# Optimization experiments

Measured on AMD Instinct MI355X. Metric: run time of the kernel, lower is better.

## Reference

```python
import jax, jax.numpy as jnp
import numpy as np

T, B, F, H = 2048, 256, 64, 128


def setup_inputs() -> dict:
    key = jax.random.key(0)
    ks = jax.random.split(key, 6)
    s_i = 1.0 / np.sqrt(F)
    s_h = 1.0 / np.sqrt(H)
    x = jax.random.normal(ks[0], (T, B, F), dtype=jnp.float32)
    # flax GRUCell params: input kernels ir/iz/in (with bias), hidden kernels
    # hr/hz (no bias), hn (with bias). Packed as [r | z | n].
    Wi = jax.random.normal(ks[1], (F, 3 * H), dtype=jnp.float32) * s_i
    bi = jnp.zeros((3 * H,), dtype=jnp.float32)
    Whrz = jax.random.normal(ks[2], (H, 2 * H), dtype=jnp.float32) * s_h  # hr | hz
    Whn = jax.random.normal(ks[3], (H, H), dtype=jnp.float32) * s_h
    bn = jnp.zeros((H,), dtype=jnp.float32)
    return {"x": x, "Wi": Wi, "bi": bi, "Whrz": Whrz, "Whn": Whn, "bn": bn}


def reference(x, Wi, bi, Whrz, Whn, bn):
    # Faithful flax nn.RNN(nn.GRUCell(H), time_major=True) with zero init carry.
    # r = sigmoid(x@Wir + bir + h@Whr)
    # z = sigmoid(x@Wiz + biz + h@Whz)
    # h' = (1 - z) * n + z * h
    Tn, Bn, _ = x.shape
    Hn = Whn.shape[0]
    # Precompute all input projections in one big GEMM (same math, vectorized over time).
    xg = jnp.einsum("tbf,fg->tbg", x, Wi) + bi  # [T, B, 3H]

    def step(h, xg_t):
        hrz = h @ Whrz  # [B, 2H]
        r = jax.nn.sigmoid(xg_t[..., :Hn] + hrz[..., :Hn])
        z = jax.nn.sigmoid(xg_t[..., Hn:2 * Hn] + hrz[..., Hn:])
        n = jnp.tanh(xg_t[..., 2 * Hn:] + r * (h @ Whn + bn))
        h_new = (1.0 - z) * n + z * h
        return h_new, h_new

    h0 = jnp.zeros((Bn, Hn), dtype=x.dtype)
    _, ys = jax.lax.scan(step, h0, xg)
    return ys  # [T, B, H] — all hidden states, as nn.RNN returns
```

## Files before the change

kernel.cpp:

```cpp
#include <hip/hip_runtime.h>

#define TT 2048
#define BB 256
#define FF 64
#define HH 128
#define NT 512
#define MR 4
#define NBLK (BB / MR)
#define RS (BB * FF / 4)
#define HSTR 320

typedef _Float16 half8 __attribute__((ext_vector_type(8)));
typedef _Float16 half4 __attribute__((ext_vector_type(4)));
typedef float    f32x4 __attribute__((ext_vector_type(4)));

#if __has_builtin(__builtin_amdgcn_rcpf)
#define FRCP(v) __builtin_amdgcn_rcpf(v)
#else
#define FRCP(v) (1.0f / (v))
#endif

__device__ __forceinline__ f32x4 mf(f32x4 a, f32x4 b, f32x4 c) {
  return __builtin_amdgcn_mfma_f32_16x16x32_f16(
      __builtin_bit_cast(half8, a), __builtin_bit_cast(half8, b), c, 0, 0, 0);
}

__device__ __forceinline__ void step_barrier() {
  asm volatile("s_waitcnt lgkmcnt(0)" ::: "memory");
  __builtin_amdgcn_s_barrier();
  __builtin_amdgcn_sched_barrier(0);
}

__global__ void __launch_bounds__(NT)
__attribute__((amdgpu_waves_per_eu(2, 2)))
gru_scan_kernel(const float* __restrict__ x,
                const float* __restrict__ Wi,
                const float* __restrict__ bi,
                const float* __restrict__ Whrz,
                const float* __restrict__ Whn,
                const float* __restrict__ bn,
                float* __restrict__ out)
{
  const int tid   = threadIdx.x;
  const int w     = tid >> 6;
  const int l     = tid & 63;
  const int n16   = l & 15;
  const int q     = l >> 4;
  const int u     = 16 * w + n16;
  const int rr    = n16 & 3;
  const int brow0 = blockIdx.x * MR;

  __shared__ __align__(16) char h_lds[2][MR * HSTR];
  __shared__ __align__(16) char x_lds[4][MR * HSTR];

  f32x4 Bhr[4], Bhz[4], Bhn2[4];
  f32x4 Bxr[2], Bxz[2], Bxn2[2];
  #pragma unroll
  for (int kt = 0; kt < 4; ++kt) {
    half8 fr, fz, fn;
    #pragma unroll
    for (int j = 0; j < 8; ++j) {
      const int k = 32 * kt + 8 * q + j;
      fr[j] = (_Float16)Whrz[(size_t)k * 256 + u];
      fz[j] = (_Float16)Whrz[(size_t)k * 256 + 128 + u];
      fn[j] = (_Float16)Whn[(size_t)k * 128 + u];
    }
    Bhr[kt]  = __builtin_bit_cast(f32x4, fr);
    Bhz[kt]  = __builtin_bit_cast(f32x4, fz);
    Bhn2[kt] = __builtin_bit_cast(f32x4, fn);
  }
  #pragma unroll
  for (int kt = 0; kt < 2; ++kt) {
    half8 fr, fz, fn;
    #pragma unroll
    for (int j = 0; j < 8; ++j) {
      const int k = 32 * kt + 8 * q + j;
      fr[j] = (_Float16)Wi[(size_t)k * 384 + u];
      fz[j] = (_Float16)Wi[(size_t)k * 384 + 128 + u];
      fn[j] = (_Float16)Wi[(size_t)k * 384 + 256 + u];
    }
    Bxr[kt]  = __builtin_bit_cast(f32x4, fr);
    Bxz[kt]  = __builtin_bit_cast(f32x4, fz);
    Bxn2[kt] = __builtin_bit_cast(f32x4, fn);
  }
  const float bR = bi[u], bZ = bi[128 + u], bX = bi[256 + u], bH = bn[u];
  const f32x4 biasR = f32x4{bR, bR, bR, bR};
  const f32x4 biasZ = f32x4{bZ, bZ, bZ, bZ};
  const f32x4 biasX = f32x4{bX, bX, bX, bX};
  const f32x4 biasH = f32x4{bH, bH, bH, bH};

  int hA[4], xA[2];
  #pragma unroll
  for (int kt = 0; kt < 4; ++kt) hA[kt] = rr * HSTR + kt * 64 + q * 16;
  #pragma unroll
  for (int kt = 0; kt < 2; ++kt) xA[kt] = rr * HSTR + kt * 64 + q * 16;

  const int hW = q * HSTR + 2 * u;

  const bool loader = (tid < 64);
  const int  srow   = tid >> 4;
  const int  sc     = tid & 15;
  const int  sbyte  = srow * HSTR + sc * 8;

  if (loader) {
    *(f32x4*)(h_lds[0] + srow * HSTR + sc * 16) = f32x4{0.f, 0.f, 0.f, 0.f};
    #pragma unroll
    for (int s = 0; s < 2; ++s) {
      const float4 v =
          *(const float4*)(x + ((size_t)s * BB + brow0 + srow) * FF + sc * 4);
      half4 hf;
      hf[0] = (_Float16)v.x; hf[1] = (_Float16)v.y;
      hf[2] = (_Float16)v.z; hf[3] = (_Float16)v.w;
      *(half4*)(x_lds[s] + sbyte) = hf;
    }
  }
  const float4* xsrc =
      (const float4*)(x + ((size_t)2 * BB + brow0 + srow) * FF + sc * 4);
  float4 xva, xvb;
  if (loader) {
    xva = xsrc[0];
    xvb = xsrc[(size_t)RS];
    xsrc += 2 * (size_t)RS;
  }

  float h_old = 0.0f;
  float* outp = out + ((size_t)brow0 + q) * HH + u;
  __syncthreads();

#define STEP(P, XV)                                                         \
  {                                                                         \
    const int t_ = tbase + (P);                                             \
    const char* hb = h_lds[(P) & 1];                                        \
    const char* xb = x_lds[(P) & 3];                                        \
    f32x4 Ah0 = *(const f32x4*)(hb + hA[0]);                                \
    f32x4 Ah1 = *(const f32x4*)(hb + hA[1]);                                \
    f32x4 Ah2 = *(const f32x4*)(hb + hA[2]);                                \
    f32x4 Ah3 = *(const f32x4*)(hb + hA[3]);                                \
    f32x4 Ax0 = *(const f32x4*)(xb + xA[0]);                                \
    f32x4 Ax1 = *(const f32x4*)(xb + xA[1]);                                \
    if (loader) {                                                           \
      if (t_ + 2 < TT) {                                                    \
        half4 hf;                                                           \
        hf[0] = (_Float16)XV.x; hf[1] = (_Float16)XV.y;                     \
        hf[2] = (_Float16)XV.z; hf[3] = (_Float16)XV.w;                     \
        *(half4*)(x_lds[((P) + 2) & 3] + sbyte) = hf;           \
      }                                                                     \
      if (t_ + 4 < TT) { XV = *xsrc; xsrc += RS; }              \
    }                                                                       \
    f32x4 Cr = mf(Ah0, Bhr[0], biasR);                                      \
    Cr = mf(Ah1, Bhr[1], Cr); Cr = mf(Ah2, Bhr[2], Cr);                     \
    Cr = mf(Ah3, Bhr[3], Cr);                                               \
    Cr = mf(Ax0, Bxr[0], Cr); Cr = mf(Ax1, Bxr[1], Cr);                     \
    f32x4 Cz = mf(Ah0, Bhz[0], biasZ);                                      \
    Cz = mf(Ah1, Bhz[1], Cz); Cz = mf(Ah2, Bhz[2], Cz);                     \
    Cz = mf(Ah3, Bhz[3], Cz);                                               \
    Cz = mf(Ax0, Bxz[0], Cz); Cz = mf(Ax1, Bxz[1], Cz);                     \
    f32x4 Chn = mf(Ah0, Bhn2[0], biasH);                                    \
    Chn = mf(Ah1, Bhn2[1], Chn); Chn = mf(Ah2, Bhn2[2], Chn);               \
    Chn = mf(Ah3, Bhn2[3], Chn);                                            \
    f32x4 Cxn = mf(Ax0, Bxn2[0], biasX);                                    \
    Cxn = mf(Ax1, Bxn2[1], Cxn);                                            \
    \
    \
    const float cr  = (q < 2) ? ((q == 0) ? Cr[0]  : Cr[1])                 \
                              : ((q == 2) ? Cr[2]  : Cr[3]);                \
    const float cz  = (q < 2) ? ((q == 0) ? Cz[0]  : Cz[1])                 \
                              : ((q == 2) ? Cz[2]  : Cz[3]);                \
    const float chn = (q < 2) ? ((q == 0) ? Chn[0] : Chn[1])                \
                              : ((q == 2) ? Chn[2] : Chn[3]);               \
    const float cxn = (q < 2) ? ((q == 0) ? Cxn[0] : Cxn[1])                \
                              : ((q == 2) ? Cxn[2] : Cxn[3]);               \
    const float A_ = __expf(-cr);                                           \
    const float rg = FRCP(1.0f + A_);                                       \
    const float B_ = __expf(-cz);                                           \
    const float na = cxn + rg * chn;                                        \
    const float E_ = __expf(2.0f * na);                                     \
    const float Ep1 = E_ + 1.0f;                                            \
    const float num = h_old * Ep1 + B_ * (E_ - 1.0f);                       \
    const float hv  = num * FRCP(Ep1 * (1.0f + B_));                        \
    h_old = hv;                                                             \
    *(_Float16*)(h_lds[((P) + 1) & 1] + hW) = (_Float16)hv;                 \
    *outp = hv;                                                             \
    outp += (size_t)BB * HH;                                                \
    step_barrier();                                                         \
  }

  for (int tbase = 0; tbase < TT; tbase += 4) {
    STEP(0, xva)
    STEP(1, xvb)
    STEP(2, xva)
    STEP(3, xvb)
  }
#undef STEP
}

extern "C" void kernel_launch(void* const* d_in, const int* in_sizes, int n_in,
                              void* d_out, int out_size, void* d_ws, size_t ws_size,
                              hipStream_t stream) {
  const float* x    = (const float*)d_in[0];
  const float* Wi   = (const float*)d_in[1];
  const float* bi   = (const float*)d_in[2];
  const float* Whrz = (const float*)d_in[3];
  const float* Whn  = (const float*)d_in[4];
  const float* bn   = (const float*)d_in[5];
  float* out = (float*)d_out;

  gru_scan_kernel<<<dim3(NBLK), dim3(NT), 0, stream>>>(
      x, Wi, bi, Whrz, Whn, bn, out);
}
```

Measured before the change: 893.7 us.

## Process eight batch rows per block with two MFMA tiles per wave

Doubles the batch rows handled per block from 4 to 8, so each wave runs two sets of MFMA chains and gate computations per timestep. The grid halves to 32 blocks, and each block pays its per-step barrier and weight-load setup once for twice the work. Biases move from the MFMA accumulator init into the scalar gate math, so the accumulators start at zero. The trade is a longer serial critical path per step and fewer CUs in use, which only pays off if the latency is hidden by interleaving the two independent MFMA chains.

After: 1.720 ms. 92.5% more time.

```diff
diff --git a/kernel.cpp b/kernel.cpp
--- a/kernel.cpp
+++ b/kernel.cpp
@@ -5,7 +5,7 @@
 #define FF 64
 #define HH 128
 #define NT 512
-#define MR 4
+#define MR 8
 #define NBLK (BB / MR)
 #define RS (BB * FF / 4)
 #define HSTR 320
@@ -84,26 +84,23 @@
     Bxn2[kt] = __builtin_bit_cast(f32x4, fn);
   }
   const float bR = bi[u], bZ = bi[128 + u], bX = bi[256 + u], bH = bn[u];
-  const f32x4 biasR = f32x4{bR, bR, bR, bR};
-  const f32x4 biasZ = f32x4{bZ, bZ, bZ, bZ};
-  const f32x4 biasX = f32x4{bX, bX, bX, bX};
-  const f32x4 biasH = f32x4{bH, bH, bH, bH};
+  const f32x4 Zf = f32x4{0.f, 0.f, 0.f, 0.f};
 
   int hA[4], xA[2];
   #pragma unroll
   for (int kt = 0; kt < 4; ++kt) hA[kt] = rr * HSTR + kt * 64 + q * 16;
   #pragma unroll
   for (int kt = 0; kt < 2; ++kt) xA[kt] = rr * HSTR + kt * 64 + q * 16;
-
-  const int hW = q * HSTR + 2 * u;
-
-  const bool loader = (tid < 64);
+  const int hWA = q * HSTR + 2 * u;
+  const int hWB = (q + 4) * HSTR + 2 * u;
+
+  const bool loader = (tid < 128);
   const int  srow   = tid >> 4;
   const int  sc     = tid & 15;
   const int  sbyte  = srow * HSTR + sc * 8;
 
   if (loader) {
-    *(f32x4*)(h_lds[0] + srow * HSTR + sc * 16) = f32x4{0.f, 0.f, 0.f, 0.f};
+    *(f32x4*)(h_lds[0] + srow * HSTR + sc * 16) = Zf;
     #pragma unroll
     for (int s = 0; s < 2; ++s) {
       const float4 v =
@@ -123,21 +120,64 @@
     xsrc += 2 * (size_t)RS;
   }
 
-  float h_old = 0.0f;
-  float* outp = out + ((size_t)brow0 + q) * HH + u;
+  float h_oldA = 0.0f;
+  float h_oldB = 0.0f;
+  float* outpA = out + ((size_t)brow0 + q) * HH + u;
+  float* outpB = outpA + 4 * HH;
   __syncthreads();
+
+#define SEL(C_) ((q < 2) ? ((q == 0) ? (C_)[0] : (C_)[1])                   \
+                         : ((q == 2) ? (C_)[2] : (C_)[3]))
+#define GATE(cr_, cz_, chn_, cxn_, hold_, hdst_, hW_, outp_)                \
+  {                                                                         \
+    const float A_ = __expf(-((cr_) + bR));                                 \
+    const float rg = FRCP(1.0f + A_);                                       \
+    const float B_ = __expf(-((cz_) + bZ));                                 \
+    const float na = ((cxn_) + bX) + rg * ((chn_) + bH);                    \
+    const float E_ = __expf(2.0f * na);                                     \
+    const float Ep1 = E_ + 1.0f;                                            \
+    const float num = (hold_) * Ep1 + B_ * (E_ - 1.0f);                     \
+    const float hv  = num * FRCP(Ep1 * (1.0f + B_));                        \
+    (hold_) = hv;                                                           \
+    *(_Float16*)((hdst_) + (hW_)) = (_Float16)hv;                           \
+    *(outp_) = hv;                                                          \
+  }
+
+#define GEMM(Ah0, Ah1, Ah2, Ah3, Ax0, Ax1, Cr, Cz, Chn, Cxn)               \
+    f32x4 Cr = mf(Ah0, Bhr[0], Zf);                                         \
+    Cr = mf(Ah1, Bhr[1], Cr); Cr = mf(Ah2, Bhr[2], Cr);                     \
+    Cr = mf(Ah3, Bhr[3], Cr);                                               \
+    Cr = mf(Ax0, Bxr[0], Cr); Cr = mf(Ax1, Bxr[1], Cr);                     \
+    f32x4 Cz = mf(Ah0, Bhz[0], Zf);                                         \
+    Cz = mf(Ah1, Bhz[1], Cz); Cz = mf(Ah2, Bhz[2], Cz);                     \
+    Cz = mf(Ah3, Bhz[3], Cz);                                               \
+    Cz = mf(Ax0, Bxz[0], Cz); Cz = mf(Ax1, Bxz[1], Cz);                     \
+    f32x4 Chn = mf(Ah0, Bhn2[0], Zf);                                       \
+    Chn = mf(Ah1, Bhn2[1], Chn); Chn = mf(Ah2, Bhn2[2], Chn);               \
+    Chn = mf(Ah3, Bhn2[3], Chn);                                            \
+    f32x4 Cxn = mf(Ax0, Bxn2[0], Zf);                                       \
+    Cxn = mf(Ax1, Bxn2[1], Cxn);
 
 #define STEP(P, XV)                                                         \
   {                                                                         \
     const int t_ = tbase + (P);                                             \
     const char* hb = h_lds[(P) & 1];                                        \
     const char* xb = x_lds[(P) & 3];                                        \
-    f32x4 Ah0 = *(const f32x4*)(hb + hA[0]);                                \
-    f32x4 Ah1 = *(const f32x4*)(hb + hA[1]);                                \
-    f32x4 Ah2 = *(const f32x4*)(hb + hA[2]);                                \
-    f32x4 Ah3 = *(const f32x4*)(hb + hA[3]);                                \
-    f32x4 Ax0 = *(const f32x4*)(xb + xA[0]);                                \
-    f32x4 Ax1 = *(const f32x4*)(xb + xA[1]);                                \
+    char* hdst = h_lds[((P) + 1) & 1];                                      \
+                                          \
+    f32x4 aAh0 = *(const f32x4*)(hb + hA[0]);                               \
+    f32x4 aAh1 = *(const f32x4*)(hb + hA[1]);                               \
+    f32x4 aAh2 = *(const f32x4*)(hb + hA[2]);                               \
+    f32x4 aAh3 = *(const f32x4*)(hb + hA[3]);                               \
+    f32x4 aAx0 = *(const f32x4*)(xb + xA[0]);                               \
+    f32x4 aAx1 = *(const f32x4*)(xb + xA[1]);                               \
+                                          \
+    f32x4 bAh0 = *(const f32x4*)(hb + 4 * HSTR + hA[0]);                    \
+    f32x4 bAh1 = *(const f32x4*)(hb + 4 * HSTR + hA[1]);                    \
+    f32x4 bAh2 = *(const f32x4*)(hb + 4 * HSTR + hA[2]);                    \
+    f32x4 bAh3 = *(const f32x4*)(hb + 4 * HSTR + hA[3]);                    \
+    f32x4 bAx0 = *(const f32x4*)(xb + 4 * HSTR + xA[0]);                    \
+    f32x4 bAx1 = *(const f32x4*)(xb + 4 * HSTR + xA[1]);                    \
     if (loader) {                                                           \
       if (t_ + 2 < TT) {                                                    \
         half4 hf;                                                           \
@@ -147,41 +187,13 @@
       }                                                                     \
       if (t_ + 4 < TT) { XV = *xsrc; xsrc += RS; }              \
     }                                                                       \
-    f32x4 Cr = mf(Ah0, Bhr[0], biasR);                                      \
-    Cr = mf(Ah1, Bhr[1], Cr); Cr = mf(Ah2, Bhr[2], Cr);                     \
-    Cr = mf(Ah3, Bhr[3], Cr);                                               \
-    Cr = mf(Ax0, Bxr[0], Cr); Cr = mf(Ax1, Bxr[1], Cr);                     \
-    f32x4 Cz = mf(Ah0, Bhz[0], biasZ);                                      \
-    Cz = mf(Ah1, Bhz[1], Cz); Cz = mf(Ah2, Bhz[2], Cz);                     \
-    Cz = mf(Ah3, Bhz[3], Cz);                                               \
-    Cz = mf(Ax0, Bxz[0], Cz); Cz = mf(Ax1, Bxz[1], Cz);                     \
-    f32x4 Chn = mf(Ah0, Bhn2[0], biasH);                                    \
-    Chn = mf(Ah1, Bhn2[1], Chn); Chn = mf(Ah2, Bhn2[2], Chn);               \
-    Chn = mf(Ah3, Bhn2[3], Chn);                                            \
-    f32x4 Cxn = mf(Ax0, Bxn2[0], biasX);                                    \
-    Cxn = mf(Ax1, Bxn2[1], Cxn);                                            \
-    \
-    \
-    const float cr  = (q < 2) ? ((q == 0) ? Cr[0]  : Cr[1])                 \
-                              : ((q == 2) ? Cr[2]  : Cr[3]);                \
-    const float cz  = (q < 2) ? ((q == 0) ? Cz[0]  : Cz[1])                 \
-                              : ((q == 2) ? Cz[2]  : Cz[3]);                \
-    const float chn = (q < 2) ? ((q == 0) ? Chn[0] : Chn[1])                \
-                              : ((q == 2) ? Chn[2] : Chn[3]);               \
-    const float cxn = (q < 2) ? ((q == 0) ? Cxn[0] : Cxn[1])                \
-                              : ((q == 2) ? Cxn[2] : Cxn[3]);               \
-    const float A_ = __expf(-cr);                                           \
-    const float rg = FRCP(1.0f + A_);                                       \
-    const float B_ = __expf(-cz);                                           \
-    const float na = cxn + rg * chn;                                        \
-    const float E_ = __expf(2.0f * na);                                     \
-    const float Ep1 = E_ + 1.0f;                                            \
-    const float num = h_old * Ep1 + B_ * (E_ - 1.0f);                       \
-    const float hv  = num * FRCP(Ep1 * (1.0f + B_));                        \
-    h_old = hv;                                                             \
-    *(_Float16*)(h_lds[((P) + 1) & 1] + hW) = (_Float16)hv;                 \
-    *outp = hv;                                                             \
-    outp += (size_t)BB * HH;                                                \
+           \
+    GEMM(aAh0, aAh1, aAh2, aAh3, aAx0, aAx1, CrA, CzA, ChnA, CxnA)          \
+    GEMM(bAh0, bAh1, bAh2, bAh3, bAx0, bAx1, CrB, CzB, ChnB, CxnB)          \
+    GATE(SEL(CrA), SEL(CzA), SEL(ChnA), SEL(CxnA), h_oldA, hdst, hWA, outpA)\
+    GATE(SEL(CrB), SEL(CzB), SEL(ChnB), SEL(CxnB), h_oldB, hdst, hWB, outpB)\
+    outpA += (size_t)BB * HH;                                               \
+    outpB += (size_t)BB * HH;                                               \
     step_barrier();                                                         \
   }
 
@@ -192,6 +204,9 @@
     STEP(3, xvb)
   }
 #undef STEP
+#undef GEMM
+#undef GATE
+#undef SEL
 }
 
 extern "C" void kernel_launch(void* const* d_in, const int* in_sizes, int n_in,
```

## Load x fragments directly into registers and reorder MFMAs to start with input projection

Applied to the files above, without the earlier changes.

Removes the LDS staging of x, where one wave loaded, converted and stored x tiles for the whole block. Each lane now loads its own MFMA A-fragment of x straight from global memory two steps ahead and converts it with packed round-toward-zero f16 conversions. The MFMA chain is reordered so the x-projection products, which do not depend on the previous hidden state, are issued before the h-dependent ones and can overlap the LDS read of h. In exchange every wave issues redundant global loads of x, adds register pressure, and the conversion now rounds toward zero instead of to nearest.

Result: slower. 1.815 ms (+103.1%).

```diff
diff --git a/kernel.cpp b/kernel.cpp
--- a/kernel.cpp
+++ b/kernel.cpp
@@ -7,11 +7,10 @@
 #define NT 512
 #define MR 4
 #define NBLK (BB / MR)
-#define RS (BB * FF / 4)
 #define HSTR 320
 
 typedef _Float16 half8 __attribute__((ext_vector_type(8)));
-typedef _Float16 half4 __attribute__((ext_vector_type(4)));
+typedef __fp16   fp16x2 __attribute__((ext_vector_type(2)));
 typedef float    f32x4 __attribute__((ext_vector_type(4)));
 
 #if __has_builtin(__builtin_amdgcn_rcpf)
@@ -23,6 +22,15 @@
 __device__ __forceinline__ f32x4 mf(f32x4 a, f32x4 b, f32x4 c) {
   return __builtin_amdgcn_mfma_f32_16x16x32_f16(
       __builtin_bit_cast(half8, a), __builtin_bit_cast(half8, b), c, 0, 0, 0);
+}
+
+__device__ __forceinline__ f32x4 cvt8(const float4 a, const float4 b) {
+  union { fp16x2 h[4]; f32x4 v; } u;
+  u.h[0] = __builtin_amdgcn_cvt_pkrtz(a.x, a.y);
+  u.h[1] = __builtin_amdgcn_cvt_pkrtz(a.z, a.w);
+  u.h[2] = __builtin_amdgcn_cvt_pkrtz(b.x, b.y);
+  u.h[3] = __builtin_amdgcn_cvt_pkrtz(b.z, b.w);
+  return u.v;
 }
 
 __device__ __forceinline__ void step_barrier() {
@@ -51,7 +59,6 @@
   const int brow0 = blockIdx.x * MR;
 
   __shared__ __align__(16) char h_lds[2][MR * HSTR];
-  __shared__ __align__(16) char x_lds[4][MR * HSTR];
 
   f32x4 Bhr[4], Bhz[4], Bhn2[4];
   f32x4 Bxr[2], Bxz[2], Bxn2[2];
@@ -89,87 +96,80 @@
   const f32x4 biasX = f32x4{bX, bX, bX, bX};
   const f32x4 biasH = f32x4{bH, bH, bH, bH};
 
-  int hA[4], xA[2];
+  int hA[4];
   #pragma unroll
   for (int kt = 0; kt < 4; ++kt) hA[kt] = rr * HSTR + kt * 64 + q * 16;
-  #pragma unroll
-  for (int kt = 0; kt < 2; ++kt) xA[kt] = rr * HSTR + kt * 64 + q * 16;
-
   const int hW = q * HSTR + 2 * u;
 
-  const bool loader = (tid < 64);
-  const int  srow   = tid >> 4;
-  const int  sc     = tid & 15;
-  const int  sbyte  = srow * HSTR + sc * 8;
-
-  if (loader) {
-    *(f32x4*)(h_lds[0] + srow * HSTR + sc * 16) = f32x4{0.f, 0.f, 0.f, 0.f};
-    #pragma unroll
-    for (int s = 0; s < 2; ++s) {
-      const float4 v =
-          *(const float4*)(x + ((size_t)s * BB + brow0 + srow) * FF + sc * 4);
-      half4 hf;
-      hf[0] = (_Float16)v.x; hf[1] = (_Float16)v.y;
-      hf[2] = (_Float16)v.z; hf[3] = (_Float16)v.w;
-      *(half4*)(x_lds[s] + sbyte) = hf;
-    }
-  }
-  const float4* xsrc =
-      (const float4*)(x + ((size_t)2 * BB + brow0 + srow) * FF + sc * 4);
-  float4 xva, xvb;
-  if (loader) {
-    xva = xsrc[0];
-    xvb = xsrc[(size_t)RS];
-    xsrc += 2 * (size_t)RS;
+  const size_t xrow0 = ((size_t)brow0 + rr) * FF + q * 8;
+
+  if (tid < 64) {
+    *(f32x4*)(h_lds[0] + (tid >> 4) * HSTR + (tid & 15) * 16) =
+        f32x4{0.f, 0.f, 0.f, 0.f};
+  }
+  float4 rA0a, rA0b, rA1a, rA1b;
+  float4 rB0a, rB0b, rB1a, rB1b;
+  {
+    const float* p0 = x + xrow0;
+    rA0a = *(const float4*)(p0);
+    rA0b = *(const float4*)(p0 + 4);
+    rA1a = *(const float4*)(p0 + 32);
+    rA1b = *(const float4*)(p0 + 36);
+    const float* p1 = x + (size_t)BB * FF + xrow0;
+    rB0a = *(const float4*)(p1);
+    rB0b = *(const float4*)(p1 + 4);
+    rB1a = *(const float4*)(p1 + 32);
+    rB1b = *(const float4*)(p1 + 36);
   }
 
   float h_old = 0.0f;
   float* outp = out + ((size_t)brow0 + q) * HH + u;
   __syncthreads();
 
-#define STEP(P, XV)                                                         \
+#define SEL(C_) ((q < 2) ? ((q == 0) ? (C_)[0] : (C_)[1])                   \
+                         : ((q == 2) ? (C_)[2] : (C_)[3]))
+
+#define STEP(P, R0a, R0b, R1a, R1b)                                         \
   {                                                                         \
     const int t_ = tbase + (P);                                             \
     const char* hb = h_lds[(P) & 1];                                        \
-    const char* xb = x_lds[(P) & 3];                                        \
+    char* hdst = (char*)h_lds[((P) + 1) & 1];                               \
+             \
     f32x4 Ah0 = *(const f32x4*)(hb + hA[0]);                                \
     f32x4 Ah1 = *(const f32x4*)(hb + hA[1]);                                \
     f32x4 Ah2 = *(const f32x4*)(hb + hA[2]);                                \
     f32x4 Ah3 = *(const f32x4*)(hb + hA[3]);                                \
-    f32x4 Ax0 = *(const f32x4*)(xb + xA[0]);                                \
-    f32x4 Ax1 = *(const f32x4*)(xb + xA[1]);                                \
-    if (loader) {                                                           \
-      if (t_ + 2 < TT) {                                                    \
-        half4 hf;                                                           \
-        hf[0] = (_Float16)XV.x; hf[1] = (_Float16)XV.y;                     \
-        hf[2] = (_Float16)XV.z; hf[3] = (_Float16)XV.w;                     \
-        *(half4*)(x_lds[((P) + 2) & 3] + sbyte) = hf;           \
-      }                                                                     \
-      if (t_ + 4 < TT) { XV = *xsrc; xsrc += RS; }              \
+                     \
+    f32x4 Ax0 = cvt8(R0a, R0b);                                             \
+    f32x4 Ax1 = cvt8(R1a, R1b);                                             \
+               \
+    {                                                                       \
+      const int t2 = (t_ + 2 < TT) ? t_ + 2 : TT - 1;                       \
+      const float* p = x + (size_t)t2 * BB * FF + xrow0;                    \
+      R0a = *(const float4*)(p);                                            \
+      R0b = *(const float4*)(p + 4);                                        \
+      R1a = *(const float4*)(p + 32);                                       \
+      R1b = *(const float4*)(p + 36);                                       \
     }                                                                       \
-    f32x4 Cr = mf(Ah0, Bhr[0], biasR);                                      \
-    Cr = mf(Ah1, Bhr[1], Cr); Cr = mf(Ah2, Bhr[2], Cr);                     \
-    Cr = mf(Ah3, Bhr[3], Cr);                                               \
-    Cr = mf(Ax0, Bxr[0], Cr); Cr = mf(Ax1, Bxr[1], Cr);                     \
-    f32x4 Cz = mf(Ah0, Bhz[0], biasZ);                                      \
-    Cz = mf(Ah1, Bhz[1], Cz); Cz = mf(Ah2, Bhz[2], Cz);                     \
-    Cz = mf(Ah3, Bhz[3], Cz);                                               \
-    Cz = mf(Ax0, Bxz[0], Cz); Cz = mf(Ax1, Bxz[1], Cz);                     \
+            \
+    f32x4 Cr = mf(Ax0, Bxr[0], biasR);                                      \
+    Cr = mf(Ax1, Bxr[1], Cr);                                               \
+    f32x4 Cz = mf(Ax0, Bxz[0], biasZ);                                      \
+    Cz = mf(Ax1, Bxz[1], Cz);                                               \
+    f32x4 Cxn = mf(Ax0, Bxn2[0], biasX);                                    \
+    Cxn = mf(Ax1, Bxn2[1], Cxn);                                            \
+    Cr = mf(Ah0, Bhr[0], Cr); Cr = mf(Ah1, Bhr[1], Cr);                     \
+    Cr = mf(Ah2, Bhr[2], Cr); Cr = mf(Ah3, Bhr[3], Cr);                     \
+    Cz = mf(Ah0, Bhz[0], Cz); Cz = mf(Ah1, Bhz[1], Cz);                     \
+    Cz = mf(Ah2, Bhz[2], Cz); Cz = mf(Ah3, Bhz[3], Cz);                     \
     f32x4 Chn = mf(Ah0, Bhn2[0], biasH);                                    \
     Chn = mf(Ah1, Bhn2[1], Chn); Chn = mf(Ah2, Bhn2[2], Chn);               \
     Chn = mf(Ah3, Bhn2[3], Chn);                                            \
-    f32x4 Cxn = mf(Ax0, Bxn2[0], biasX);                                    \
-    Cxn = mf(Ax1, Bxn2[1], Cxn);                                            \
-    \
-    \
-    const float cr  = (q < 2) ? ((q == 0) ? Cr[0]  : Cr[1])                 \
-                              : ((q == 2) ? Cr[2]  : Cr[3]);                \
-    const float cz  = (q < 2) ? ((q == 0) ? Cz[0]  : Cz[1])                 \
-                              : ((q == 2) ? Cz[2]  : Cz[3]);                \
-    const float chn = (q < 2) ? ((q == 0) ? Chn[0] : Chn[1])                \
-                              : ((q == 2) ? Chn[2] : Chn[3]);               \
-    const float cxn = (q < 2) ? ((q == 0) ? Cxn[0] : Cxn[1])                \
-                              : ((q == 2) ? Cxn[2] : Cxn[3]);               \
+         \
+    const float cr  = SEL(Cr);                                              \
+    const float cz  = SEL(Cz);                                              \
+    const float chn = SEL(Chn);                                             \
+    const float cxn = SEL(Cxn);                                             \
     const float A_ = __expf(-cr);                                           \
     const float rg = FRCP(1.0f + A_);                                       \
     const float B_ = __expf(-cz);                                           \
@@ -179,19 +179,18 @@
     const float num = h_old * Ep1 + B_ * (E_ - 1.0f);                       \
     const float hv  = num * FRCP(Ep1 * (1.0f + B_));                        \
     h_old = hv;                                                             \
-    *(_Float16*)(h_lds[((P) + 1) & 1] + hW) = (_Float16)hv;                 \
+    *(_Float16*)(hdst + hW) = (_Float16)hv;                                 \
     *outp = hv;                                                             \
     outp += (size_t)BB * HH;                                                \
     step_barrier();                                                         \
   }
 
-  for (int tbase = 0; tbase < TT; tbase += 4) {
-    STEP(0, xva)
-    STEP(1, xvb)
-    STEP(2, xva)
-    STEP(3, xvb)
+  for (int tbase = 0; tbase < TT; tbase += 2) {
+    STEP(0, rA0a, rA0b, rA1a, rA1b)
+    STEP(1, rB0a, rB0b, rB1a, rB1b)
   }
 #undef STEP
+#undef SEL
 }
 
 extern "C" void kernel_launch(void* const* d_in, const int* in_sizes, int n_in,
```
